# Kernel tuning notes

Measured on AMD Instinct MI355X. Metric: run time of the kernel, lower is better.

## Reference

```python
import jax, jax.numpy as jnp
import numpy as np

KSIZE = 7   # pooled output grid (kernel_size)
SR = 2      # bilinear sampling ratio per bin side


def setup_inputs() -> dict:
    key = jax.random.key(0)
    k1, k2, k3 = jax.random.split(key, 3)
    B, H, W, C = 8, 64, 64, 256
    N = 4096
    x = jax.random.normal(k1, (B, H, W, C), jnp.float32)
    # random valid boxes in feature-map coordinates: (y1, x1, y2, x2), y2 > y1
    raw = jax.random.uniform(k2, (N, 4), jnp.float32)
    c1 = raw[:, :2] * jnp.array([H - 1.0, W - 1.0], jnp.float32)
    c2 = raw[:, 2:] * jnp.array([H - 1.0, W - 1.0], jnp.float32)
    lo = jnp.minimum(c1, c2)
    hi = jnp.maximum(c1, c2) + 1.0  # ensure non-degenerate boxes
    rois = jnp.stack([lo[:, 0], lo[:, 1], hi[:, 0], hi[:, 1]], axis=1)
    batch_idx = jax.random.randint(k3, (N,), 0, B, jnp.int32)
    return {"x": x, "rois": rois, "batch_idx": batch_idx}


def reference(x, rois, batch_idx):
    """ROIAlign: per-ROI bilinear sampling + average pooling.

    x:         [B, H, W, C] feature map (channels-last)
    rois:      [N, 4] boxes (y1, x1, y2, x2) in feature-map pixel coords
    batch_idx: [N] int index of the image each ROI belongs to
    returns:   [N, KSIZE, KSIZE, C]
    """
    B, H, W, C = x.shape
    N = rois.shape[0]
    K, S = KSIZE, KSIZE * SR  # S x S sample points per ROI

    y1, x1, y2, x2 = rois[:, 0], rois[:, 1], rois[:, 2], rois[:, 3]
    bin_h = (y2 - y1) / K
    bin_w = (x2 - x1) / K

    # sample coordinate s within ROI: y1 + (s + 0.5)/SR * bin_h, s in [0, S)
    off = (jnp.arange(S, dtype=x.dtype) + 0.5) / SR          # [S]
    sy = y1[:, None] + off[None, :] * bin_h[:, None]          # [N, S]
    sx = x1[:, None] + off[None, :] * bin_w[:, None]          # [N, S]

    yy = sy[:, :, None]                                       # [N, S, 1]
    xx = sx[:, None, :]                                       # [N, 1, S]
    y0 = jnp.clip(jnp.floor(yy), 0, H - 2).astype(jnp.int32)  # [N, S, 1]
    x0 = jnp.clip(jnp.floor(xx), 0, W - 2).astype(jnp.int32)  # [N, 1, S]
    ly = jnp.clip(yy - y0, 0.0, 1.0)                          # [N, S, 1]
    lx = jnp.clip(xx - x0, 0.0, 1.0)                          # [N, 1, S]

    b = batch_idx[:, None, None]                              # [N, 1, 1]
    # gather 4 bilinear corners -> each [N, S, S, C]
    v00 = x[b, y0, x0]
    v01 = x[b, y0, x0 + 1]
    v10 = x[b, y0 + 1, x0]
    v11 = x[b, y0 + 1, x0 + 1]

    ly_ = ly[..., None]  # [N, S, 1, 1]
    lx_ = lx[..., None]  # [N, 1, S, 1]
    val = (v00 * (1 - ly_) * (1 - lx_) + v01 * (1 - ly_) * lx_
           + v10 * ly_ * (1 - lx_) + v11 * ly_ * lx_)          # [N, S, S, C]

    # average-pool the SR x SR samples inside each of the K x K bins
    out = val.reshape(N, K, SR, K, SR, C).mean(axis=(2, 4))   # [N, K, K, C]
    return out
```

## Files before the change

kernel.cpp:

```cpp
#include <hip/hip_runtime.h>

#define KSIZE 7
#define SR    2
#define NBINS (KSIZE * KSIZE)
#define NMAX  4096
#define BMAX  8

typedef float v4f __attribute__((ext_vector_type(4)));

constexpr int C4c  = 64;
constexpr int WC4c = 4096;

__global__ __launch_bounds__(256) void bucket_kernel(
    const int* __restrict__ bi, int* __restrict__ assign, int N, int B, int cap)
{
    __shared__ int cnt[BMAX];
    __shared__ int ovf_n, ovf_c;
    __shared__ int asg[NMAX];
    __shared__ int ovf[NMAX];

    const int t = threadIdx.x;
    if (t < BMAX) cnt[t] = 0;
    if (t == 0) { ovf_n = 0; ovf_c = 0; }
    for (int i = t; i < N; i += 256) asg[i] = -1;
    __syncthreads();

    for (int i = t; i < N; i += 256) {
        int k = bi[i];
        int p = atomicAdd(&cnt[k], 1);
        if (p < cap) asg[p * B + k] = i;
        else { int q = atomicAdd(&ovf_n, 1); ovf[q] = i; }
    }
    __syncthreads();

    for (int i = t; i < N; i += 256) {
        if (asg[i] < 0) { int q = atomicAdd(&ovf_c, 1); asg[i] = ovf[q]; }
    }
    __syncthreads();

    for (int i = t; i < N; i += 256) assign[i] = asg[i];
}

__global__ __launch_bounds__(256, 3) void roialign_kernel(
    const float* __restrict__ x,
    const float* __restrict__ rois,
    const int*   __restrict__ batch_idx,
    float*       __restrict__ out,
    const int*   __restrict__ assign,
    int H, int W, int C)
{
    __shared__ int   sh_n;
    __shared__ int   ridx[KSIZE][4];
    __shared__ float rwgt[KSIZE][4];
    __shared__ int   cidx[KSIZE][4];
    __shared__ float cwgt[KSIZE][4];
    __shared__ int   rn[KSIZE];
    __shared__ int   cn[KSIZE];

    const int t = threadIdx.x;
    if (t == 0) sh_n = assign[blockIdx.x];
    __syncthreads();
    const int n = sh_n;

    const float4 rb = ((const float4*)rois)[n];
    const float bin_h = (rb.z - rb.x) / (float)KSIZE;
    const float bin_w = (rb.w - rb.y) / (float)KSIZE;

    if (t < KSIZE || (t >= 16 && t < 16 + KSIZE)) {
        const bool isrow = (t < KSIZE);
        const int  k     = isrow ? t : t - 16;
        const float base = isrow ? rb.x : rb.y;
        const float bsz  = isrow ? bin_h : bin_w;
        const int   dim  = isrow ? H : W;

        const float sA = base + ((float)k + 0.25f) * bsz;
        const float sB = base + ((float)k + 0.75f) * bsz;
        const float fA = fminf(fmaxf(floorf(sA), 0.0f), (float)(dim - 2));
        const float fB = fminf(fmaxf(floorf(sB), 0.0f), (float)(dim - 2));
        const int   iA = (int)fA,  iB = (int)fB;
        const float lA = fminf(fmaxf(sA - fA, 0.0f), 1.0f);
        const float lB = fminf(fmaxf(sB - fB, 0.0f), 1.0f);

        int   i0 = iA,     i1 = iA + 1, i2, i3, cnt_;
        float w0 = (1.0f - lA) * 0.5f, w1 = lA * 0.5f, w2, w3;
        if (iB == iA) {
            w0 += (1.0f - lB) * 0.5f;
            w1 += lB * 0.5f;
            i2 = iA; w2 = 0.0f;
            i3 = iA; w3 = 0.0f;
            cnt_ = 2;
        } else if (iB == iA + 1) {
            w1 += (1.0f - lB) * 0.5f;
            i2 = iB + 1; w2 = lB * 0.5f;
            i3 = iA;     w3 = 0.0f;
            cnt_ = 3;
        } else {
            i2 = iB;     w2 = (1.0f - lB) * 0.5f;
            i3 = iB + 1; w3 = lB * 0.5f;
            cnt_ = 4;
        }
        if (isrow) {
            ridx[k][0] = i0; ridx[k][1] = i1; ridx[k][2] = i2; ridx[k][3] = i3;
            rwgt[k][0] = w0; rwgt[k][1] = w1; rwgt[k][2] = w2; rwgt[k][3] = w3;
            rn[k] = cnt_;
        } else {
            cidx[k][0] = i0; cidx[k][1] = i1; cidx[k][2] = i2; cidx[k][3] = i3;
            cwgt[k][0] = w0; cwgt[k][1] = w1; cwgt[k][2] = w2; cwgt[k][3] = w3;
            cn[k] = cnt_;
        }
    }
    __syncthreads();

    const int bimg = batch_idx[n];
    const int lane = t & 63;
    const int wave = t >> 6;

    const v4f* __restrict__ xbase =
        (const v4f*)x + (size_t)bimg * 64 * WC4c + lane;
    float* __restrict__ outn = out + (size_t)n * NBINS * 256;

    v4f vA[16], vB[16];
    #pragma unroll
    for (int i = 0; i < 16; ++i) {
        vA[i] = (v4f){0.f, 0.f, 0.f, 0.f};
        vB[i] = (v4f){0.f, 0.f, 0.f, 0.f};
    }

#define LR2(RV, RP) V[(RV)*4+0] = (RP)[c0_]; V[(RV)*4+1] = (RP)[c1_];
#define LR3(RV, RP) LR2(RV, RP) V[(RV)*4+2] = (RP)[c2_];
#define LR4(RV, RP) LR3(RV, RP) V[(RV)*4+3] = (RP)[c3_];
#define LDN2(NC) LR##NC(0, r0_) LR##NC(1, r1_)
#define LDN3(NC) LDN2(NC) LR##NC(2, r2_)
#define LDN4(NC) LDN3(NC) LR##NC(3, r3_)

#define ISSUE(VARR, KY, KX)                                                 \
    do {                                                                    \
        v4f (&V)[16] = VARR;                                                \
        const v4f* r0_ = xbase + ridx[KY][0] * WC4c;                        \
        const v4f* r1_ = xbase + ridx[KY][1] * WC4c;                        \
        const v4f* r2_ = xbase + ridx[KY][2] * WC4c;                        \
        const v4f* r3_ = xbase + ridx[KY][3] * WC4c;                        \
        const int c0_ = cidx[KX][0] * C4c, c1_ = cidx[KX][1] * C4c;         \
        const int c2_ = cidx[KX][2] * C4c, c3_ = cidx[KX][3] * C4c;         \
        const int code_ = (rn[KY] - 2) * 3 + (cn[KX] - 2);                  \
        switch (code_) {                                                    \
        case 0: { LDN2(2) } break;                                          \
        case 1: { LDN2(3) } break;                                          \
        case 2: { LDN2(4) } break;                                          \
        case 3: { LDN3(2) } break;                                          \
        case 4: { LDN3(3) } break;                                          \
        case 5: { LDN3(4) } break;                                          \
        case 6: { LDN4(2) } break;                                          \
        case 7: { LDN4(3) } break;                                          \
        default: { LDN4(4) } break;                                         \
        }                                                                   \
    } while (0)

#define COMPUTE(VARR, BIN, KY, KX)                                          \
    do {                                                                    \
        v4f (&V)[16] = VARR;                                                \
        v4f acc = {0.f, 0.f, 0.f, 0.f};                                     \
        _Pragma("unroll")                                                   \
        for (int r_ = 0; r_ < 4; ++r_) {                                    \
            const float wr_ = rwgt[KY][r_];                                 \
            acc += V[r_*4+0] * (wr_ * cwgt[KX][0]);                         \
            acc += V[r_*4+1] * (wr_ * cwgt[KX][1]);                         \
            acc += V[r_*4+2] * (wr_ * cwgt[KX][2]);                         \
            acc += V[r_*4+3] * (wr_ * cwgt[KX][3]);                         \
        }                                                                   \
        v4f* op_ = (v4f*)(outn + (size_t)(BIN) * 256) + lane;               \
        __builtin_nontemporal_store(acc, op_);                              \
    } while (0)

    int bin = wave;
    int kyA = bin / KSIZE, kxA = bin - kyA * KSIZE;
    int kyB, kxB;
    ISSUE(vA, kyA, kxA);
    for (;;) {
        int nb = bin + 4;
        if (nb < NBINS) {
            kyB = nb / KSIZE; kxB = nb - kyB * KSIZE;
            ISSUE(vB, kyB, kxB);
            COMPUTE(vA, bin, kyA, kxA);
            bin = nb;
        } else {
            COMPUTE(vA, bin, kyA, kxA);
            break;
        }
        nb = bin + 4;
        if (nb < NBINS) {
            kyA = nb / KSIZE; kxA = nb - kyA * KSIZE;
            ISSUE(vA, kyA, kxA);
            COMPUTE(vB, bin, kyB, kxB);
            bin = nb;
        } else {
            COMPUTE(vB, bin, kyB, kxB);
            break;
        }
    }
#undef ISSUE
#undef COMPUTE
#undef LR2
#undef LR3
#undef LR4
#undef LDN2
#undef LDN3
#undef LDN4
}

extern "C" void kernel_launch(void* const* d_in, const int* in_sizes, int n_in,
                              void* d_out, int out_size, void* d_ws, size_t ws_size,
                              hipStream_t stream) {
    const float* x         = (const float*)d_in[0];
    const float* rois      = (const float*)d_in[1];
    const int*   batch_idx = (const int*)d_in[2];
    float*       out       = (float*)d_out;
    int*         assign    = (int*)d_ws;

    const int H = 64, W = 64, C = 256;
    const int N = in_sizes[1] / 4;
    const int B = in_sizes[0] / (H * W * C);
    const int cap = N / B;

    bucket_kernel<<<1, 256, 0, stream>>>(batch_idx, assign, N, B, cap);
    roialign_kernel<<<N, 256, 0, stream>>>(x, rois, batch_idx, out, assign,
                                           H, W, C);
}
```

Measured before the change: 297.8 us.

## Process four ROIs per block with shared setup and a continuous bin pipeline

```diff
diff --git a/kernel.cpp b/kernel.cpp
--- a/kernel.cpp
+++ b/kernel.cpp
@@ -1,10 +1,10 @@
 #include <hip/hip_runtime.h>
 
 #define KSIZE 7
-#define SR    2
 #define NBINS (KSIZE * KSIZE)
 #define NMAX  4096
 #define BMAX  8
+#define RPB   4
 
 typedef float v4f __attribute__((ext_vector_type(4)));
 
@@ -49,75 +49,83 @@
     const int*   __restrict__ assign,
     int H, int W, int C)
 {
-    __shared__ int   sh_n;
-    __shared__ int   ridx[KSIZE][4];
-    __shared__ float rwgt[KSIZE][4];
-    __shared__ int   cidx[KSIZE][4];
-    __shared__ float cwgt[KSIZE][4];
-    __shared__ int   rn[KSIZE];
-    __shared__ int   cn[KSIZE];
-
-    const int t = threadIdx.x;
-    if (t == 0) sh_n = assign[blockIdx.x];
-    __syncthreads();
-    const int n = sh_n;
-
-    const float4 rb = ((const float4*)rois)[n];
-    const float bin_h = (rb.z - rb.x) / (float)KSIZE;
-    const float bin_w = (rb.w - rb.y) / (float)KSIZE;
-
-    if (t < KSIZE || (t >= 16 && t < 16 + KSIZE)) {
-        const bool isrow = (t < KSIZE);
-        const int  k     = isrow ? t : t - 16;
-        const float base = isrow ? rb.x : rb.y;
-        const float bsz  = isrow ? bin_h : bin_w;
-        const int   dim  = isrow ? H : W;
-
-        const float sA = base + ((float)k + 0.25f) * bsz;
-        const float sB = base + ((float)k + 0.75f) * bsz;
-        const float fA = fminf(fmaxf(floorf(sA), 0.0f), (float)(dim - 2));
-        const float fB = fminf(fmaxf(floorf(sB), 0.0f), (float)(dim - 2));
-        const int   iA = (int)fA,  iB = (int)fB;
-        const float lA = fminf(fmaxf(sA - fA, 0.0f), 1.0f);
-        const float lB = fminf(fmaxf(sB - fB, 0.0f), 1.0f);
-
-        int   i0 = iA,     i1 = iA + 1, i2, i3, cnt_;
-        float w0 = (1.0f - lA) * 0.5f, w1 = lA * 0.5f, w2, w3;
-        if (iB == iA) {
-            w0 += (1.0f - lB) * 0.5f;
-            w1 += lB * 0.5f;
-            i2 = iA; w2 = 0.0f;
-            i3 = iA; w3 = 0.0f;
-            cnt_ = 2;
-        } else if (iB == iA + 1) {
-            w1 += (1.0f - lB) * 0.5f;
-            i2 = iB + 1; w2 = lB * 0.5f;
-            i3 = iA;     w3 = 0.0f;
-            cnt_ = 3;
-        } else {
-            i2 = iB;     w2 = (1.0f - lB) * 0.5f;
-            i3 = iB + 1; w3 = lB * 0.5f;
-            cnt_ = 4;
+    __shared__ int   sh_n[RPB];
+    __shared__ int   sh_b[RPB];
+    __shared__ int   ridx[RPB][KSIZE][4];
+    __shared__ float rwgt[RPB][KSIZE][4];
+    __shared__ int   cidx[RPB][KSIZE][4];
+    __shared__ float cwgt[RPB][KSIZE][4];
+    __shared__ int   rn[RPB][KSIZE];
+    __shared__ int   cn[RPB][KSIZE];
+
+    const int t   = threadIdx.x;
+    const int img = blockIdx.x & 7;
+    const int grp = blockIdx.x >> 3;
+    if (t < RPB) sh_n[t] = assign[(grp * RPB + t) * 8 + img];
+    __syncthreads();
+
+    if (t < 16 * RPB) {
+        const int j   = t >> 4;
+        const int sub = t & 15;
+        const int n   = sh_n[j];
+        if (sub == 7) sh_b[j] = batch_idx[n];
+        const bool isrow = (sub < KSIZE);
+        const bool iscol = (sub >= 8) && (sub < 8 + KSIZE);
+        if (isrow || iscol) {
+            const float4 rb = ((const float4*)rois)[n];
+            const float bin_h = (rb.z - rb.x) / (float)KSIZE;
+            const float bin_w = (rb.w - rb.y) / (float)KSIZE;
+            const int   k    = isrow ? sub : sub - 8;
+            const float base = isrow ? rb.x : rb.y;
+            const float bsz  = isrow ? bin_h : bin_w;
+            const int   dim  = isrow ? H : W;
+
+            const float sA = base + ((float)k + 0.25f) * bsz;
+            const float sB = base + ((float)k + 0.75f) * bsz;
+            const float fA = fminf(fmaxf(floorf(sA), 0.0f), (float)(dim - 2));
+            const float fB = fminf(fmaxf(floorf(sB), 0.0f), (float)(dim - 2));
+            const int   iA = (int)fA,  iB = (int)fB;
+            const float lA = fminf(fmaxf(sA - fA, 0.0f), 1.0f);
+            const float lB = fminf(fmaxf(sB - fB, 0.0f), 1.0f);
+
+            int   i0 = iA,     i1 = iA + 1, i2, i3, cnt_;
+            float w0 = (1.0f - lA) * 0.5f, w1 = lA * 0.5f, w2, w3;
+            if (iB == iA) {
+                w0 += (1.0f - lB) * 0.5f;
+                w1 += lB * 0.5f;
+                i2 = iA; w2 = 0.0f;
+                i3 = iA; w3 = 0.0f;
+                cnt_ = 2;
+            } else if (iB == iA + 1) {
+                w1 += (1.0f - lB) * 0.5f;
+                i2 = iB + 1; w2 = lB * 0.5f;
+                i3 = iA;     w3 = 0.0f;
+                cnt_ = 3;
+            } else {
+                i2 = iB;     w2 = (1.0f - lB) * 0.5f;
+                i3 = iB + 1; w3 = lB * 0.5f;
+                cnt_ = 4;
+            }
+            if (isrow) {
+                ridx[j][k][0] = i0; ridx[j][k][1] = i1;
+                ridx[j][k][2] = i2; ridx[j][k][3] = i3;
+                rwgt[j][k][0] = w0; rwgt[j][k][1] = w1;
+                rwgt[j][k][2] = w2; rwgt[j][k][3] = w3;
+                rn[j][k] = cnt_;
+            } else {
+                cidx[j][k][0] = i0; cidx[j][k][1] = i1;
+                cidx[j][k][2] = i2; cidx[j][k][3] = i3;
+                cwgt[j][k][0] = w0; cwgt[j][k][1] = w1;
+                cwgt[j][k][2] = w2; cwgt[j][k][3] = w3;
+                cn[j][k] = cnt_;
+            }
         }
-        if (isrow) {
-            ridx[k][0] = i0; ridx[k][1] = i1; ridx[k][2] = i2; ridx[k][3] = i3;
-            rwgt[k][0] = w0; rwgt[k][1] = w1; rwgt[k][2] = w2; rwgt[k][3] = w3;
-            rn[k] = cnt_;
-        } else {
-            cidx[k][0] = i0; cidx[k][1] = i1; cidx[k][2] = i2; cidx[k][3] = i3;
-            cwgt[k][0] = w0; cwgt[k][1] = w1; cwgt[k][2] = w2; cwgt[k][3] = w3;
-            cn[k] = cnt_;
-        }
-    }
-    __syncthreads();
-
-    const int bimg = batch_idx[n];
+    }
+    __syncthreads();
+
     const int lane = t & 63;
     const int wave = t >> 6;
-
-    const v4f* __restrict__ xbase =
-        (const v4f*)x + (size_t)bimg * 64 * WC4c + lane;
-    float* __restrict__ outn = out + (size_t)n * NBINS * 256;
+    const v4f* __restrict__ xv = (const v4f*)x;
 
     v4f vA[16], vB[16];
     #pragma unroll
@@ -133,16 +141,17 @@
 #define LDN3(NC) LDN2(NC) LR##NC(2, r2_)
 #define LDN4(NC) LDN3(NC) LR##NC(3, r3_)
 
-#define ISSUE(VARR, KY, KX)                                                 \
+#define ISSUE(VARR, J, KY, KX)                                              \
     do {                                                                    \
         v4f (&V)[16] = VARR;                                                \
-        const v4f* r0_ = xbase + ridx[KY][0] * WC4c;                        \
-        const v4f* r1_ = xbase + ridx[KY][1] * WC4c;                        \
-        const v4f* r2_ = xbase + ridx[KY][2] * WC4c;                        \
-        const v4f* r3_ = xbase + ridx[KY][3] * WC4c;                        \
-        const int c0_ = cidx[KX][0] * C4c, c1_ = cidx[KX][1] * C4c;         \
-        const int c2_ = cidx[KX][2] * C4c, c3_ = cidx[KX][3] * C4c;         \
-        const int code_ = (rn[KY] - 2) * 3 + (cn[KX] - 2);                  \
+        const v4f* xbase_ = xv + (size_t)sh_b[J] * 64 * WC4c + lane;        \
+        const v4f* r0_ = xbase_ + ridx[J][KY][0] * WC4c;                    \
+        const v4f* r1_ = xbase_ + ridx[J][KY][1] * WC4c;                    \
+        const v4f* r2_ = xbase_ + ridx[J][KY][2] * WC4c;                    \
+        const v4f* r3_ = xbase_ + ridx[J][KY][3] * WC4c;                    \
+        const int c0_ = cidx[J][KX][0] * C4c, c1_ = cidx[J][KX][1] * C4c;   \
+        const int c2_ = cidx[J][KX][2] * C4c, c3_ = cidx[J][KX][3] * C4c;   \
+        const int code_ = (rn[J][KY] - 2) * 3 + (cn[J][KX] - 2);            \
         switch (code_) {                                                    \
         case 0: { LDN2(2) } break;                                          \
         case 1: { LDN2(3) } break;                                          \
@@ -156,50 +165,61 @@
         }                                                                   \
     } while (0)
 
-#define COMPUTE(VARR, BIN, KY, KX)                                          \
+#define COMPUTE(VARR, J, KY, KX)                                            \
     do {                                                                    \
         v4f (&V)[16] = VARR;                                                \
         v4f acc = {0.f, 0.f, 0.f, 0.f};                                     \
         _Pragma("unroll")                                                   \
         for (int r_ = 0; r_ < 4; ++r_) {                                    \
-            const float wr_ = rwgt[KY][r_];                                 \
-            acc += V[r_*4+0] * (wr_ * cwgt[KX][0]);                         \
-            acc += V[r_*4+1] * (wr_ * cwgt[KX][1]);                         \
-            acc += V[r_*4+2] * (wr_ * cwgt[KX][2]);                         \
-            acc += V[r_*4+3] * (wr_ * cwgt[KX][3]);                         \
+            const float wr_ = rwgt[J][KY][r_];                              \
+            acc += V[r_*4+0] * (wr_ * cwgt[J][KX][0]);                      \
+            acc += V[r_*4+1] * (wr_ * cwgt[J][KX][1]);                      \
+            acc += V[r_*4+2] * (wr_ * cwgt[J][KX][2]);                      \
+            acc += V[r_*4+3] * (wr_ * cwgt[J][KX][3]);                      \
         }                                                                   \
-        v4f* op_ = (v4f*)(outn + (size_t)(BIN) * 256) + lane;               \
+        v4f* op_ = (v4f*)(out + (size_t)sh_n[J] * (NBINS * 256)             \
+                              + (size_t)((KY) * KSIZE + (KX)) * 256) + lane;\
         __builtin_nontemporal_store(acc, op_);                              \
     } while (0)
 
-    int bin = wave;
-    int kyA = bin / KSIZE, kxA = bin - kyA * KSIZE;
-    int kyB, kxB;
-    ISSUE(vA, kyA, kxA);
+#define ADV(J, KY, KX)                                                      \
+    do {                                                                    \
+        KX += 4;                                                            \
+        if (KX >= KSIZE) {                                                  \
+            KX -= KSIZE;                                                    \
+            if (++KY >= KSIZE) { KY -= KSIZE; ++J; }                        \
+        }                                                                   \
+    } while (0)
+
+    int jA = 0, kyA = 0, kxA = wave;
+    int jB, kyB, kxB;
+    int g = wave;
+    ISSUE(vA, jA, kyA, kxA);
     for (;;) {
-        int nb = bin + 4;
-        if (nb < NBINS) {
-            kyB = nb / KSIZE; kxB = nb - kyB * KSIZE;
-            ISSUE(vB, kyB, kxB);
-            COMPUTE(vA, bin, kyA, kxA);
-            bin = nb;
+        int gn = g + 4;
+        if (gn < RPB * NBINS) {
+            jB = jA; kyB = kyA; kxB = kxA; ADV(jB, kyB, kxB);
+            ISSUE(vB, jB, kyB, kxB);
+            COMPUTE(vA, jA, kyA, kxA);
+            g = gn;
         } else {
-            COMPUTE(vA, bin, kyA, kxA);
+            COMPUTE(vA, jA, kyA, kxA);
             break;
         }
-        nb = bin + 4;
-        if (nb < NBINS) {
-            kyA = nb / KSIZE; kxA = nb - kyA * KSIZE;
-            ISSUE(vA, kyA, kxA);
-            COMPUTE(vB, bin, kyB, kxB);
-            bin = nb;
+        gn = g + 4;
+        if (gn < RPB * NBINS) {
+            jA = jB; kyA = kyB; kxA = kxB; ADV(jA, kyA, kxA);
+            ISSUE(vA, jA, kyA, kxA);
+            COMPUTE(vB, jB, kyB, kxB);
+            g = gn;
         } else {
-            COMPUTE(vB, bin, kyB, kxB);
+            COMPUTE(vB, jB, kyB, kxB);
             break;
         }
     }
 #undef ISSUE
 #undef COMPUTE
+#undef ADV
 #undef LR2
 #undef LR3
 #undef LR4
@@ -223,6 +243,6 @@
     const int cap = N / B;
 
     bucket_kernel<<<1, 256, 0, stream>>>(batch_idx, assign, N, B, cap);
-    roialign_kernel<<<N, 256, 0, stream>>>(x, rois, batch_idx, out, assign,
-                                           H, W, C);
+    roialign_kernel<<<N / RPB, 256, 0, stream>>>(x, rois, batch_idx, out,
+                                                 assign, H, W, C);
 }
```

Result: slower. 511.1 us (+71.6%).
